# Optimization experiments

Measured on AMD Instinct MI355X. Metric: run time of the kernel, lower is better.

## Reference

```python
import jax, jax.numpy as jnp
import numpy as np
import math

NUM_HEADS = 16
HIDDEN = 1024
HEAD_DIM = HIDDEN // NUM_HEADS
WIN = 512  # relative position window size
B, S = 2, 2048
LN_EPS = 1e-5


def setup_inputs() -> dict:
    key = jax.random.key(0)
    ks = jax.random.split(key, 8)
    sd = 1.0 / math.sqrt(HIDDEN)
    return {
        "x": jax.random.normal(ks[0], (B, S, HIDDEN), jnp.float32),
        "Wq": jax.random.normal(ks[1], (HIDDEN, HIDDEN), jnp.float32) * sd,
        "bq": jnp.zeros((HIDDEN,), jnp.float32),
        "Wk": jax.random.normal(ks[2], (HIDDEN, HIDDEN), jnp.float32) * sd,
        "bk": jnp.zeros((HIDDEN,), jnp.float32),
        "Wv": jax.random.normal(ks[3], (HIDDEN, HIDDEN), jnp.float32) * sd,
        "bv": jnp.zeros((HIDDEN,), jnp.float32),
        "Wo": jax.random.normal(ks[4], (HIDDEN, HIDDEN), jnp.float32) * sd,
        "bo": jnp.zeros((HIDDEN,), jnp.float32),
        "relpos_table": jax.random.normal(ks[5], (WIN, HIDDEN), jnp.float32),
        "ln_gamma": jnp.ones((HIDDEN,), jnp.float32),
        "ln_beta": jnp.zeros((HIDDEN,), jnp.float32),
        "Wrk": jax.random.normal(ks[6], (HIDDEN, HIDDEN), jnp.float32) * sd,
        "brk": jnp.zeros((HIDDEN,), jnp.float32),
        "Wrq": jax.random.normal(ks[7], (HIDDEN, HIDDEN), jnp.float32) * sd,
        "brq": jnp.zeros((HIDDEN,), jnp.float32),
    }


def reference(x, Wq, bq, Wk, bk, Wv, bv, Wo, bo,
              relpos_table, ln_gamma, ln_beta, Wrk, brk, Wrq, brq):
    Bsz, Slen, H = x.shape
    nh, hd = NUM_HEADS, HEAD_DIM

    # QKV projections -> [B, S, nh, hd]
    q = (x @ Wq + bq).reshape(Bsz, Slen, nh, hd)
    k = (x @ Wk + bk).reshape(Bsz, Slen, nh, hd)
    v = (x @ Wv + bv).reshape(Bsz, Slen, nh, hd)

    mu = relpos_table.mean(-1, keepdims=True)
    var = relpos_table.var(-1, keepdims=True)  # biased, as in torch LayerNorm
    e = (relpos_table - mu) * jax.lax.rsqrt(var + LN_EPS) * ln_gamma + ln_beta

    # relative position index matrix [S, S]: clamp(key - query, -W+1, 0) + W-1
    qi = jnp.arange(Slen)
    relpos = jnp.clip(qi[None, :] - qi[:, None], -WIN + 1, 0) + (WIN - 1)

    rk = (e @ Wrk + brk).reshape(WIN, nh, hd)
    rq = (e @ Wrq + brq).reshape(WIN, nh, hd)

    # content-to-content scores [B, nh, S, S]
    c2c = jnp.einsum('bqhd,bkhd->bhqk', q, k)

    # content-to-position: scores over window then gather along window axis
    qps = jnp.einsum('bnhd,whd->bhnw', q, rk)           # [B, nh, S, W]
    c2p = qps[:, :, qi[:, None], relpos]                # [B, nh, S, S]

    # position-to-content: window x key_seq scores, gather along window axis
    kps = jnp.einsum('bnhd,whd->bhwn', k, rq)           # [B, nh, W, S]
    p2c = kps[:, :, relpos, qi[None, :]]                # [B, nh, S, S]

    scale_factor = 3.0  # 1 + relpos_q_enabled + relpos_k_enabled
    logits = (c2c + c2p + p2c) / math.sqrt(hd * scale_factor)

    # causal mask
    causal = qi[None, :] <= qi[:, None]
    logits = jnp.where(causal[None, None], logits, jnp.finfo(logits.dtype).min)

    attn = jax.nn.softmax(logits, axis=-1)              # [B, nh, S, S]
    out = jnp.einsum('bhqk,bkhd->bqhd', attn, v).reshape(Bsz, Slen, H)
    return out @ Wo + bo
```

## Files before the change

kernel.cpp:

```cpp
#include <hip/hip_runtime.h>
#include <math.h>

#define NH 16
#define HD 64
#define HID 1024
#define SEQ 2048
#define NB 2

typedef __attribute__((ext_vector_type(8))) short short8;
typedef __attribute__((ext_vector_type(4))) float f32x4;
typedef unsigned short u16;
typedef unsigned int u32;

constexpr float LN_EPS_C = 1e-5f;
constexpr float SM_SCALE = 0.07216878364870323f;

__device__ inline u16 f2b(float f) {
  unsigned u = __builtin_bit_cast(unsigned, f);
  u = (u + 0x7FFFu + ((u >> 16) & 1u)) >> 16;
  return (u16)u;
}
__device__ inline float b2f(u16 h) {
  unsigned u = ((unsigned)h) << 16;
  return __builtin_bit_cast(float, u);
}
__device__ inline u32 pk2(float lo, float hi) {
  return (u32)f2b(lo) | ((u32)f2b(hi) << 16);
}
__device__ inline f32x4 mfma16(short8 a, short8 b, f32x4 c) {
  return __builtin_amdgcn_mfma_f32_16x16x32_bf16(a, b, c, 0, 0, 0);
}
__device__ inline short8 swz8(const u16* base, int row, int hc) {
  return *reinterpret_cast<const short8*>(&base[row * 64 + 8 * (hc ^ (row & 7))]);
}
__device__ inline int vrot(int row, int col) {
  return row * 72 + ((col + 16 * ((row >> 3) & 3)) & 63);
}
template <int N>
__device__ inline float rorf(float x) {
  return __builtin_bit_cast(float,
      __builtin_amdgcn_update_dpp(0, __builtin_bit_cast(int, x),
                                  0x120 + N, 0xF, 0xF, true));
}
__device__ inline float rmax16(float x) {
  x = fmaxf(x, rorf<1>(x)); x = fmaxf(x, rorf<2>(x));
  x = fmaxf(x, rorf<4>(x)); x = fmaxf(x, rorf<8>(x));
  return x;
}
__device__ inline float rsum16(float x) {
  x += rorf<1>(x); x += rorf<2>(x); x += rorf<4>(x); x += rorf<8>(x);
  return x;
}

__global__ __launch_bounds__(256) void ln_kernel(const float* __restrict__ tbl,
    const float* __restrict__ gamma, const float* __restrict__ beta,
    u16* __restrict__ e) {
  int row = blockIdx.x;
  int t = threadIdx.x;
  const float4* rp = reinterpret_cast<const float4*>(tbl + (size_t)row * HID);
  float4 x = rp[t];
  float s = x.x + x.y + x.z + x.w;
  float ss = x.x * x.x + x.y * x.y + x.z * x.z + x.w * x.w;
  #pragma unroll
  for (int o = 1; o < 64; o <<= 1) {
    s += __shfl_xor(s, o);
    ss += __shfl_xor(ss, o);
  }
  __shared__ float sb[4], ssb[4];
  int w = t >> 6;
  if ((t & 63) == 0) { sb[w] = s; ssb[w] = ss; }
  __syncthreads();
  s = sb[0] + sb[1] + sb[2] + sb[3];
  ss = ssb[0] + ssb[1] + ssb[2] + ssb[3];
  float mu = s * (1.0f / HID);
  float var = ss * (1.0f / HID) - mu * mu;
  float rs = rsqrtf(var + LN_EPS_C);
  float4 g = reinterpret_cast<const float4*>(gamma)[t];
  float4 bt = reinterpret_cast<const float4*>(beta)[t];
  ushort4 o4;
  o4.x = f2b((x.x - mu) * rs * g.x + bt.x);
  o4.y = f2b((x.y - mu) * rs * g.y + bt.y);
  o4.z = f2b((x.z - mu) * rs * g.z + bt.z);
  o4.w = f2b((x.w - mu) * rs * g.w + bt.w);
  *reinterpret_cast<ushort4*>(&e[(size_t)row * HID + t * 4]) = o4;
}

__global__ __launch_bounds__(256) void conv_bf16(const float* __restrict__ src,
    u16* __restrict__ dst, int n) {
  int i = (blockIdx.x * 256 + threadIdx.x) * 8;
  if (i >= n) return;
  float4 a = *reinterpret_cast<const float4*>(&src[i]);
  float4 c = *reinterpret_cast<const float4*>(&src[i + 4]);
  short8 o;
  o[0] = (short)f2b(a.x); o[1] = (short)f2b(a.y); o[2] = (short)f2b(a.z); o[3] = (short)f2b(a.w);
  o[4] = (short)f2b(c.x); o[5] = (short)f2b(c.y); o[6] = (short)f2b(c.z); o[7] = (short)f2b(c.w);
  *reinterpret_cast<short8*>(&dst[i]) = o;
}

struct P6 {
  const float* s[6];
  u16* d[6];
};
__global__ __launch_bounds__(256) void transp_all(P6 p) {
  __shared__ float T[32][33];
  const float* W = p.s[blockIdx.z];
  u16* Wt = p.d[blockIdx.z];
  int bn = blockIdx.x * 32, bk = blockIdx.y * 32;
  int t = threadIdx.x;
  int r = t >> 3, c4 = (t & 7) * 4;
  float4 v = *reinterpret_cast<const float4*>(&W[(size_t)(bk + r) * HID + bn + c4]);
  T[r][c4 + 0] = v.x; T[r][c4 + 1] = v.y; T[r][c4 + 2] = v.z; T[r][c4 + 3] = v.w;
  __syncthreads();
  int n = t >> 3, k4 = (t & 7) * 4;
  ushort4 o;
  o.x = f2b(T[k4 + 0][n]); o.y = f2b(T[k4 + 1][n]);
  o.z = f2b(T[k4 + 2][n]); o.w = f2b(T[k4 + 3][n]);
  *reinterpret_cast<ushort4*>(&Wt[(size_t)(bn + n) * HID + bk + k4]) = o;
}

struct GO {
  const float* bias[3];
  void* out[3];
};
template <bool F32OUT>
__global__ __launch_bounds__(512) void gemm_bf16(const u16* __restrict__ A,
    const u16* __restrict__ Bt, GO go) {
  __shared__ u16 Al[8192];
  __shared__ u16 Bl[8192];
  int t = threadIdx.x;
  int cb = blockIdx.x * 128, rb = blockIdx.y * 128;
  int which = cb >> 10, cbl = cb & 1023;
  const float* bias = go.bias[which];
  void* Cout = go.out[which];
  int wv = t >> 6, lane = t & 63, l15 = lane & 15, lg = lane >> 4;
  int wr = (wv >> 2) * 64, wc = (wv & 3) * 32;
  int srow = t >> 2, sch = t & 3;
  f32x4 acc[4][2];
  #pragma unroll
  for (int i = 0; i < 4; ++i)
    #pragma unroll
    for (int j = 0; j < 2; ++j) acc[i][j] = (f32x4){0.f, 0.f, 0.f, 0.f};
  const u16* Ap = A + (size_t)(rb + srow) * HID;
  const u16* Bp = Bt + (size_t)(cb + srow) * HID;
  int slot0 = 8 * (sch ^ (srow & 7));
  int slot1 = 8 * ((sch + 4) ^ (srow & 7));
  short8 pa0 = *reinterpret_cast<const short8*>(&Ap[sch * 8]);
  short8 pa1 = *reinterpret_cast<const short8*>(&Ap[(sch + 4) * 8]);
  short8 pb0 = *reinterpret_cast<const short8*>(&Bp[sch * 8]);
  short8 pb1 = *reinterpret_cast<const short8*>(&Bp[(sch + 4) * 8]);
  for (int kk = 0; kk < HID; kk += 64) {
    __syncthreads();
    *reinterpret_cast<short8*>(&Al[srow * 64 + slot0]) = pa0;
    *reinterpret_cast<short8*>(&Al[srow * 64 + slot1]) = pa1;
    *reinterpret_cast<short8*>(&Bl[srow * 64 + slot0]) = pb0;
    *reinterpret_cast<short8*>(&Bl[srow * 64 + slot1]) = pb1;
    __syncthreads();
    if (kk + 64 < HID) {
      pa0 = *reinterpret_cast<const short8*>(&Ap[kk + 64 + sch * 8]);
      pa1 = *reinterpret_cast<const short8*>(&Ap[kk + 64 + (sch + 4) * 8]);
      pb0 = *reinterpret_cast<const short8*>(&Bp[kk + 64 + sch * 8]);
      pb1 = *reinterpret_cast<const short8*>(&Bp[kk + 64 + (sch + 4) * 8]);
    }
    #pragma unroll
    for (int s = 0; s < 2; ++s) {
      short8 am[4], bn[2];
      #pragma unroll
      for (int i = 0; i < 4; ++i) am[i] = swz8(Al, wr + i * 16 + l15, s * 4 + lg);
      #pragma unroll
      for (int j = 0; j < 2; ++j) bn[j] = swz8(Bl, wc + j * 16 + l15, s * 4 + lg);
      #pragma unroll
      for (int i = 0; i < 4; ++i)
        #pragma unroll
        for (int j = 0; j < 2; ++j)
          acc[i][j] = mfma16(am[i], bn[j], acc[i][j]);
    }
  }
  #pragma unroll
  for (int j = 0; j < 2; ++j) {
    float bv = bias[cbl + wc + j * 16 + l15];
    #pragma unroll
    for (int i = 0; i < 4; ++i) {
      #pragma unroll
      for (int r = 0; r < 4; ++r) {
        size_t idx = (size_t)(rb + wr + i * 16 + lg * 4 + r) * HID + cbl + wc + j * 16 + l15;
        float v = acc[i][j][r] + bv;
        if (F32OUT) reinterpret_cast<float*>(Cout)[idx] = v;
        else reinterpret_cast<u16*>(Cout)[idx] = f2b(v);
      }
    }
  }
}

__global__ __launch_bounds__(256) void biasqk(const u16* __restrict__ Qb,
    const u16* __restrict__ Kb, const u16* __restrict__ RKb,
    const u16* __restrict__ RQb, float* __restrict__ qrk0,
    float* __restrict__ krq0) {
  int o = blockIdx.x * 64 + (threadIdx.x >> 2);
  int sub = threadIdx.x & 3;
  int b = o >> 15, h = (o >> 11) & 15, i = o & 2047;
  size_t rbase = (size_t)(b * SEQ + i) * HID + h * HD + sub * 16;
  size_t tbase = (size_t)h * HD + sub * 16;
  float s1 = 0.f, s2 = 0.f;
  #pragma unroll
  for (int c = 0; c < 2; ++c) {
    short8 qv = *reinterpret_cast<const short8*>(&Qb[rbase + c * 8]);
    short8 rv = *reinterpret_cast<const short8*>(&RKb[tbase + c * 8]);
    short8 kv = *reinterpret_cast<const short8*>(&Kb[rbase + c * 8]);
    short8 uv = *reinterpret_cast<const short8*>(&RQb[tbase + c * 8]);
    #pragma unroll
    for (int j = 0; j < 8; ++j) {
      s1 += b2f((u16)qv[j]) * b2f((u16)rv[j]);
      s2 += b2f((u16)kv[j]) * b2f((u16)uv[j]);
    }
  }
  s1 += __shfl_xor(s1, 1); s1 += __shfl_xor(s1, 2);
  s2 += __shfl_xor(s2, 1); s2 += __shfl_xor(s2, 2);
  if (sub == 0) { qrk0[o] = s1 * SM_SCALE; krq0[o] = s2 * SM_SCALE; }
}

__global__ __launch_bounds__(256, 3) void bias_kernel(
    const u16* __restrict__ Qb, const u16* __restrict__ Kb,
    const u16* __restrict__ RKb, const u16* __restrict__ RQb,
    u16* __restrict__ bandT) {
  __shared__ u16 smem[20992];
  const int KsO = 0, UO = 4096;
  const int RKO = UO, RQO = UO + 8192;
  const int G1O = UO, G2O = UO + 8448;

  int qt = blockIdx.x;
  int h = blockIdx.y, b = blockIdx.z;
  int q0 = qt * 64;
  int t = threadIdx.x;
  int wv = t >> 6, lane = t & 63, l15 = lane & 15, lg = lane >> 4;
  int qs = q0 + wv * 16;
  int hoff = h * HD;

  size_t qgrow = (size_t)(b * SEQ + qs + l15) * HID + hoff;
  short8 aq0 = *reinterpret_cast<const short8*>(&Qb[qgrow + lg * 8]);
  short8 aq1 = *reinterpret_cast<const short8*>(&Qb[qgrow + 32 + lg * 8]);

  const f32x4 Z = (f32x4){0.f, 0.f, 0.f, 0.f};
  int vr = t >> 2, vc8 = (t & 3) * 8;
  int ktlo = qt - 8; if (ktlo < 0) ktlo = 0;
  size_t tbase = (((size_t)(b * NH + h) * 32 + qt) * 9) << 12;

  for (int kt = ktlo; kt <= qt; ++kt) {
    int k0 = kt * 64;
    int dt = qt - kt;
    int wlo = 448 - 64 * dt; if (wlo < 0) wlo = 0;
    __syncthreads();
    {
      const u16* kg = &Kb[(size_t)(b * SEQ + k0 + vr) * HID + hoff];
      int c0 = vc8 >> 3;
      *reinterpret_cast<short8*>(&smem[KsO + vr * 64 + 8 * (c0 ^ (vr & 7))]) =
          *reinterpret_cast<const short8*>(&kg[vc8]);
      *reinterpret_cast<short8*>(&smem[KsO + vr * 64 + 8 * ((c0 + 4) ^ (vr & 7))]) =
          *reinterpret_cast<const short8*>(&kg[vc8 + 32]);
    }
    for (int e2 = t; e2 < 1024; e2 += 256) {
      int rr = e2 >> 3, cch = e2 & 7;
      int wr2 = wlo + rr; if (wr2 > 511) wr2 = 511;
      size_t gb = (size_t)wr2 * HID + hoff + cch * 8;
      int slot = 8 * (cch ^ (rr & 7));
      *reinterpret_cast<short8*>(&smem[RKO + rr * 64 + slot]) =
          *reinterpret_cast<const short8*>(&RKb[gb]);
      *reinterpret_cast<short8*>(&smem[RQO + rr * 64 + slot]) =
          *reinterpret_cast<const short8*>(&RQb[gb]);
    }
    __syncthreads();
    u32 g1p[16], g2p[16];
    #pragma unroll
    for (int cw = 0; cw < 8; ++cw) {
      short8 r0 = swz8(&smem[RKO], cw * 16 + l15, lg);
      short8 r1 = swz8(&smem[RKO], cw * 16 + l15, 4 + lg);
      f32x4 g = mfma16(r1, aq1, mfma16(r0, aq0, Z));
      g1p[2 * cw] = pk2(g[0], g[1]);
      g1p[2 * cw + 1] = pk2(g[2], g[3]);
    }
    short8 kw0 = swz8(&smem[KsO], wv * 16 + l15, lg);
    short8 kw1 = swz8(&smem[KsO], wv * 16 + l15, 4 + lg);
    #pragma unroll
    for (int cw = 0; cw < 8; ++cw) {
      short8 u0 = swz8(&smem[RQO], cw * 16 + l15, lg);
      short8 u1 = swz8(&smem[RQO], cw * 16 + l15, 4 + lg);
      f32x4 g = mfma16(u1, kw1, mfma16(u0, kw0, Z));
      g2p[2 * cw] = pk2(g[0], g[1]);
      g2p[2 * cw + 1] = pk2(g[2], g[3]);
    }
    __syncthreads();
    #pragma unroll
    for (int cw = 0; cw < 8; ++cw) {
      *reinterpret_cast<uint2*>(&smem[G1O + (wv * 16 + l15) * 132 + cw * 16 + lg * 4]) =
          make_uint2(g1p[2 * cw], g1p[2 * cw + 1]);
      *reinterpret_cast<uint2*>(&smem[G2O + (wv * 16 + l15) * 132 + cw * 16 + lg * 4]) =
          make_uint2(g2p[2 * cw], g2p[2 * cw + 1]);
    }
    __syncthreads();
    u16* outp = bandT + tbase + ((size_t)dt << 12) + t * 16;
    #pragma unroll
    for (int c = 0; c < 4; ++c) {
      float vv[4];
      #pragma unroll
      for (int r = 0; r < 4; ++r) {
        int q = qs + lg * 4 + r;
        int k = k0 + c * 16 + l15;
        int wi = 511 - (q - k) - wlo; if (wi < 0) wi = 0;
        vv[r] = (b2f(smem[G1O + (wv * 16 + lg * 4 + r) * 132 + wi]) +
                 b2f(smem[G2O + (c * 16 + l15) * 132 + wi])) * SM_SCALE;
      }
      *reinterpret_cast<uint2*>(outp + c * 4) =
          make_uint2(pk2(vv[0], vv[1]), pk2(vv[2], vv[3]));
    }
  }
}

__global__ __launch_bounds__(256, 2) void attn_mfma(
    const u16* __restrict__ Qb, const u16* __restrict__ Kb,
    const u16* __restrict__ Vb, const float* __restrict__ qrk0,
    const float* __restrict__ krq0, const u16* __restrict__ bandT,
    u16* __restrict__ ATT) {
  __shared__ u16 smem[22016];
  const int KsB[2] = {0, 4096};
  const int VtB[2] = {8192, 12800};
  const int PsO = 17408;

  int qtA = 31 - (int)blockIdx.x;
  int qtB = (int)blockIdx.x;
  int h = blockIdx.y, b = blockIdx.z;
  int t = threadIdx.x;
  int wv = t >> 6, lane = t & 63, l15 = lane & 15, lg = lane >> 4;
  int hoff = h * HD;
  int bh = (b * NH + h) * SEQ;
  size_t tbaseA = (((size_t)(b * NH + h) * 32 + qtA) * 9) << 12;
  size_t tbaseB = (((size_t)(b * NH + h) * 32 + qtB) * 9) << 12;

  int qsA = qtA * 64 + wv * 16;
  int qsB = qtB * 64 + wv * 16;
  size_t qgA = (size_t)(b * SEQ + qsA + l15) * HID + hoff;
  size_t qgB = (size_t)(b * SEQ + qsB + l15) * HID + hoff;
  short8 aqA0 = *reinterpret_cast<const short8*>(&Qb[qgA + lg * 8]);
  short8 aqA1 = *reinterpret_cast<const short8*>(&Qb[qgA + 32 + lg * 8]);
  short8 aqB0 = *reinterpret_cast<const short8*>(&Qb[qgB + lg * 8]);
  short8 aqB1 = *reinterpret_cast<const short8*>(&Qb[qgB + 32 + lg * 8]);
  float qb0A[4], qb0B[4];
  #pragma unroll
  for (int r = 0; r < 4; ++r) {
    qb0A[r] = qrk0[bh + qsA + lg * 4 + r];
    qb0B[r] = qrk0[bh + qsB + lg * 4 + r];
  }

  float mA[4], lA[4], mB[4], lB[4];
  f32x4 oA[4], oB[4];
  #pragma unroll
  for (int r = 0; r < 4; ++r) { mA[r] = -INFINITY; lA[r] = 0.f; mB[r] = -INFINITY; lB[r] = 0.f; }
  #pragma unroll
  for (int c = 0; c < 4; ++c) {
    oA[c] = (f32x4){0.f, 0.f, 0.f, 0.f};
    oB[c] = (f32x4){0.f, 0.f, 0.f, 0.f};
  }

  const f32x4 Z = (f32x4){0.f, 0.f, 0.f, 0.f};
  int vr = t >> 2, vc8 = (t & 3) * 8;
  int c0s = vc8 >> 3;
  int kslot0 = vr * 64 + 8 * (c0s ^ (vr & 7));
  int kslot1 = vr * 64 + 8 * ((c0s + 4) ^ (vr & 7));
  int vslot[16];
  #pragma unroll
  for (int j = 0; j < 8; ++j) {
    vslot[j] = vrot(vc8 + j, vr);
    vslot[8 + j] = vrot(vc8 + 32 + j, vr);
  }

  {
    const u16* kg = &Kb[(size_t)(b * SEQ + vr) * HID + hoff];
    short8 k0v = *reinterpret_cast<const short8*>(&kg[vc8]);
    short8 k1v = *reinterpret_cast<const short8*>(&kg[vc8 + 32]);
    *reinterpret_cast<short8*>(&smem[KsB[0] + kslot0]) = k0v;
    *reinterpret_cast<short8*>(&smem[KsB[0] + kslot1]) = k1v;
    const u16* vg = &Vb[(size_t)(b * SEQ + vr) * HID + hoff];
    short8 v0v = *reinterpret_cast<const short8*>(&vg[vc8]);
    short8 v1v = *reinterpret_cast<const short8*>(&vg[vc8 + 32]);
    #pragma unroll
    for (int j = 0; j < 8; ++j) smem[VtB[0] + vslot[j]] = (u16)v0v[j];
    #pragma unroll
    for (int j = 0; j < 8; ++j) smem[VtB[0] + vslot[8 + j]] = (u16)v1v[j];
  }
  __syncthreads();

  int cur = 0;
  for (int kt = 0; kt <= qtA; ++kt) {
    int k0 = kt * 64;
    int dtA = qtA - kt;
    bool doB = (kt <= qtB);
    int dtB = qtB - kt;
    bool bandedA = (dtA <= 8);
    bool bandedB = doB && (dtB <= 8);
    int ksb = KsB[cur], vtb = VtB[cur];
    int ksn = KsB[cur ^ 1], vtn = VtB[cur ^ 1];

    short8 pA0, pA1, pB0, pB1;
    if (bandedA) {
      const u16* tb = bandT + tbaseA + ((size_t)dtA << 12) + t * 16;
      pA0 = *reinterpret_cast<const short8*>(tb);
      pA1 = *reinterpret_cast<const short8*>(tb + 8);
    }
    if (bandedB) {
      const u16* tb = bandT + tbaseB + ((size_t)dtB << 12) + t * 16;
      pB0 = *reinterpret_cast<const short8*>(tb);
      pB1 = *reinterpret_cast<const short8*>(tb + 8);
    }
    float kq[4];
    if (dtA > 8 || (doB && dtB > 8)) {
      #pragma unroll
      for (int c = 0; c < 4; ++c) kq[c] = krq0[bh + k0 + c * 16 + l15];
    }
    short8 nk0, nk1, nv0, nv1;
    if (kt < qtA) {
      const u16* kg = &Kb[(size_t)(b * SEQ + k0 + 64 + vr) * HID + hoff];
      nk0 = *reinterpret_cast<const short8*>(&kg[vc8]);
      nk1 = *reinterpret_cast<const short8*>(&kg[vc8 + 32]);
      const u16* vg = &Vb[(size_t)(b * SEQ + k0 + 64 + vr) * HID + hoff];
      nv0 = *reinterpret_cast<const short8*>(&vg[vc8]);
      nv1 = *reinterpret_cast<const short8*>(&vg[vc8 + 32]);
    }

    short8 kb0[4], kb1[4];
    #pragma unroll
    for (int c = 0; c < 4; ++c) {
      kb0[c] = swz8(&smem[ksb], c * 16 + l15, lg);
      kb1[c] = swz8(&smem[ksb], c * 16 + l15, 4 + lg);
    }
    f32x4 sA[4], sB[4];
    #pragma unroll
    for (int c = 0; c < 4; ++c)
      sA[c] = mfma16(aqA1, kb1[c], mfma16(aqA0, kb0[c], Z));
    if (doB) {
      #pragma unroll
      for (int c = 0; c < 4; ++c)
        sB[c] = mfma16(aqB1, kb1[c], mfma16(aqB0, kb0[c], Z));
    }
    #pragma unroll
    for (int c = 0; c < 4; ++c) {
      #pragma unroll
      for (int r = 0; r < 4; ++r) {
        float bbv = bandedA ? b2f((u16)((c < 2 ? pA0 : pA1)[(c & 1) * 4 + r]))
                            : qb0A[r] + kq[c];
        float v = fmaf(sA[c][r], SM_SCALE, bbv);
        if (dtA == 0) {
          int ql = wv * 16 + lg * 4 + r, kl = c * 16 + l15;
          if (ql < kl) v = -INFINITY;
        }
        sA[c][r] = v;
      }
    }
    if (doB) {
      #pragma unroll
      for (int c = 0; c < 4; ++c) {
        #pragma unroll
        for (int r = 0; r < 4; ++r) {
          float bbv = bandedB ? b2f((u16)((c < 2 ? pB0 : pB1)[(c & 1) * 4 + r]))
                              : qb0B[r] + kq[c];
          float v = fmaf(sB[c][r], SM_SCALE, bbv);
          if (dtB == 0) {
            int ql = wv * 16 + lg * 4 + r, kl = c * 16 + l15;
            if (ql < kl) v = -INFINITY;
          }
          sB[c][r] = v;
        }
      }
    }
    float alA[4], alB[4];
    #pragma unroll
    for (int r = 0; r < 4; ++r) {
      float mx = fmaxf(fmaxf(sA[0][r], sA[1][r]), fmaxf(sA[2][r], sA[3][r]));
      mx = rmax16(mx);
      float mn = fmaxf(mA[r], mx);
      alA[r] = __expf(mA[r] - mn);
      float ps = 0.f;
      #pragma unroll
      for (int c = 0; c < 4; ++c) {
        float p = __expf(sA[c][r] - mn);
        sA[c][r] = p;
        ps += p;
      }
      ps = rsum16(ps);
      lA[r] = lA[r] * alA[r] + ps;
      mA[r] = mn;
    }
    if (doB) {
      #pragma unroll
      for (int r = 0; r < 4; ++r) {
        float mx = fmaxf(fmaxf(sB[0][r], sB[1][r]), fmaxf(sB[2][r], sB[3][r]));
        mx = rmax16(mx);
        float mn = fmaxf(mB[r], mx);
        alB[r] = __expf(mB[r] - mn);
        float ps = 0.f;
        #pragma unroll
        for (int c = 0; c < 4; ++c) {
          float p = __expf(sB[c][r] - mn);
          sB[c][r] = p;
          ps += p;
        }
        ps = rsum16(ps);
        lB[r] = lB[r] * alB[r] + ps;
        mB[r] = mn;
      }
    }
    short8 vb0[4], vb1[4];
    #pragma unroll
    for (int c = 0; c < 4; ++c) {
      int n = c * 16 + l15;
      vb0[c] = *reinterpret_cast<const short8*>(&smem[vtb + vrot(n, lg * 8)]);
      vb1[c] = *reinterpret_cast<const short8*>(&smem[vtb + vrot(n, 32 + lg * 8)]);
    }
    #pragma unroll
    for (int c = 0; c < 4; ++c) {
      #pragma unroll
      for (int r = 0; r < 4; ++r) {
        smem[PsO + vrot(wv * 16 + lg * 4 + r, c * 16 + l15)] = f2b(sA[c][r]);
        oA[c][r] *= alA[r];
      }
    }
    int prow = wv * 16 + l15;
    {
      short8 ap0 = *reinterpret_cast<const short8*>(&smem[PsO + vrot(prow, lg * 8)]);
      short8 ap1 = *reinterpret_cast<const short8*>(&smem[PsO + vrot(prow, 32 + lg * 8)]);
      #pragma unroll
      for (int c = 0; c < 4; ++c)
        oA[c] = mfma16(ap1, vb1[c], mfma16(ap0, vb0[c], oA[c]));
    }
    if (doB) {
      #pragma unroll
      for (int c = 0; c < 4; ++c) {
        #pragma unroll
        for (int r = 0; r < 4; ++r) {
          smem[PsO + vrot(wv * 16 + lg * 4 + r, c * 16 + l15)] = f2b(sB[c][r]);
          oB[c][r] *= alB[r];
        }
      }
      short8 bp0 = *reinterpret_cast<const short8*>(&smem[PsO + vrot(prow, lg * 8)]);
      short8 bp1 = *reinterpret_cast<const short8*>(&smem[PsO + vrot(prow, 32 + lg * 8)]);
      #pragma unroll
      for (int c = 0; c < 4; ++c)
        oB[c] = mfma16(bp1, vb1[c], mfma16(bp0, vb0[c], oB[c]));
    }
    if (kt < qtA) {
      *reinterpret_cast<short8*>(&smem[ksn + kslot0]) = nk0;
      *reinterpret_cast<short8*>(&smem[ksn + kslot1]) = nk1;
      #pragma unroll
      for (int j = 0; j < 8; ++j) smem[vtn + vslot[j]] = (u16)nv0[j];
      #pragma unroll
      for (int j = 0; j < 8; ++j) smem[vtn + vslot[8 + j]] = (u16)nv1[j];
    }
    __syncthreads();
    cur ^= 1;
  }
  #pragma unroll
  for (int r = 0; r < 4; ++r) { lA[r] = 1.0f / lA[r]; lB[r] = 1.0f / lB[r]; }
  #pragma unroll
  for (int c = 0; c < 4; ++c) {
    #pragma unroll
    for (int r = 0; r < 4; ++r) {
      size_t obA = (size_t)(b * SEQ + qsA + lg * 4 + r) * HID + hoff + c * 16 + l15;
      ATT[obA] = f2b(oA[c][r] * lA[r]);
      size_t obB = (size_t)(b * SEQ + qsB + lg * 4 + r) * HID + hoff + c * 16 + l15;
      ATT[obB] = f2b(oB[c][r] * lB[r]);
    }
  }
}

extern "C" void kernel_launch(void* const* d_in, const int* in_sizes, int n_in,
                              void* d_out, int out_size, void* d_ws, size_t ws_size,
                              hipStream_t stream) {
  const float* x      = (const float*)d_in[0];
  const float* Wq     = (const float*)d_in[1];
  const float* bq     = (const float*)d_in[2];
  const float* Wk     = (const float*)d_in[3];
  const float* bk     = (const float*)d_in[4];
  const float* Wv     = (const float*)d_in[5];
  const float* bv     = (const float*)d_in[6];
  const float* Wo     = (const float*)d_in[7];
  const float* bo     = (const float*)d_in[8];
  const float* relpos = (const float*)d_in[9];
  const float* gamma  = (const float*)d_in[10];
  const float* beta   = (const float*)d_in[11];
  const float* Wrk    = (const float*)d_in[12];
  const float* brk    = (const float*)d_in[13];
  const float* Wrq    = (const float*)d_in[14];
  const float* brq    = (const float*)d_in[15];
  float* out = (float*)d_out;

  u16* wsu = (u16*)d_ws;
  size_t off = 0;
  auto alloc = [&](size_t n) { u16* p = wsu + off; off += n; return p; };
  u16* xb   = alloc(4194304);
  u16* Eb   = alloc(524288);
  u16* WtQ  = alloc(1048576);
  u16* WtK  = alloc(1048576);
  u16* WtV  = alloc(1048576);
  u16* WtO  = alloc(1048576);
  u16* WtRK = alloc(1048576);
  u16* WtRQ = alloc(1048576);
  u16* Qb2  = alloc(4194304);
  u16* Kb2  = alloc(4194304);
  u16* Vb2  = alloc(4194304);
  u16* ATTb = alloc(4194304);
  u16* RKb2 = alloc(524288);
  u16* RQb2 = alloc(524288);
  float* qrk0 = (float*)(wsu + off); off += 131072;
  float* krq0 = (float*)(wsu + off); off += 131072;
  u16* bandT = alloc((size_t)NB * NH * 32 * 9 * 4096);

  ln_kernel<<<512, 256, 0, stream>>>(relpos, gamma, beta, Eb);
  conv_bf16<<<2048, 256, 0, stream>>>(x, xb, 4194304);
  P6 p6;
  p6.s[0] = Wq; p6.s[1] = Wk; p6.s[2] = Wv; p6.s[3] = Wo; p6.s[4] = Wrk; p6.s[5] = Wrq;
  p6.d[0] = WtQ; p6.d[1] = WtK; p6.d[2] = WtV; p6.d[3] = WtO; p6.d[4] = WtRK; p6.d[5] = WtRQ;
  dim3 gT(32, 32, 6);
  transp_all<<<gT, 256, 0, stream>>>(p6);

  GO goQKV = {{bq, bk, bv}, {Qb2, Kb2, Vb2}};
  dim3 gQKV(24, 32);
  gemm_bf16<false><<<gQKV, 512, 0, stream>>>(xb, WtQ, goQKV);
  GO goRel = {{brk, brq, brq}, {RKb2, RQb2, RQb2}};
  dim3 gRel2(16, 4);
  gemm_bf16<false><<<gRel2, 512, 0, stream>>>(Eb, WtRK, goRel);

  biasqk<<<1024, 256, 0, stream>>>(Qb2, Kb2, RKb2, RQb2, qrk0, krq0);

  dim3 gB(32, NH, NB);
  bias_kernel<<<gB, 256, 0, stream>>>(Qb2, Kb2, RKb2, RQb2, bandT);

  dim3 gA(16, NH, NB);
  attn_mfma<<<gA, 256, 0, stream>>>(Qb2, Kb2, Vb2, qrk0, krq0, bandT, ATTb);

  GO goOut = {{bo, bo, bo}, {out, out, out}};
  dim3 gBig(8, 32);
  gemm_bf16<true><<<gBig, 512, 0, stream>>>(ATTb, WtO, goOut);
}
```

Measured before the change: 218.9 us.

## Split attention key loop across two blocks and merge partial softmax results

Each attention block now handles every other key tile, selected by a split index taken from blockIdx.x, so the attention grid doubles from 512 to 1024 blocks. Each block writes unnormalized fp32 partial outputs plus its per-row max and sum to a workspace buffer. A new merge kernel combines the two halves with a log-sum-exp rescale and writes the bf16 attention output. The aim is more blocks in flight for better CU occupancy and latency hiding, at the cost of extra global traffic for the fp32 partials and one more kernel launch.

```diff
diff --git a/kernel.cpp b/kernel.cpp
--- a/kernel.cpp
+++ b/kernel.cpp
@@ -318,14 +318,16 @@
     const u16* __restrict__ Qb, const u16* __restrict__ Kb,
     const u16* __restrict__ Vb, const float* __restrict__ qrk0,
     const float* __restrict__ krq0, const u16* __restrict__ bandT,
-    u16* __restrict__ ATT) {
+    float* __restrict__ part) {
   __shared__ u16 smem[22016];
   const int KsB[2] = {0, 4096};
   const int VtB[2] = {8192, 12800};
   const int PsO = 17408;
 
-  int qtA = 31 - (int)blockIdx.x;
-  int qtB = (int)blockIdx.x;
+  int pr = (int)blockIdx.x >> 1;
+  int sp = (int)blockIdx.x & 1;
+  int qtA = 31 - pr;
+  int qtB = pr;
   int h = blockIdx.y, b = blockIdx.z;
   int t = threadIdx.x;
   int wv = t >> 6, lane = t & 63, l15 = lane & 15, lg = lane >> 4;
@@ -372,12 +374,12 @@
   }
 
   {
-    const u16* kg = &Kb[(size_t)(b * SEQ + vr) * HID + hoff];
+    const u16* kg = &Kb[(size_t)(b * SEQ + sp * 64 + vr) * HID + hoff];
     short8 k0v = *reinterpret_cast<const short8*>(&kg[vc8]);
     short8 k1v = *reinterpret_cast<const short8*>(&kg[vc8 + 32]);
     *reinterpret_cast<short8*>(&smem[KsB[0] + kslot0]) = k0v;
     *reinterpret_cast<short8*>(&smem[KsB[0] + kslot1]) = k1v;
-    const u16* vg = &Vb[(size_t)(b * SEQ + vr) * HID + hoff];
+    const u16* vg = &Vb[(size_t)(b * SEQ + sp * 64 + vr) * HID + hoff];
     short8 v0v = *reinterpret_cast<const short8*>(&vg[vc8]);
     short8 v1v = *reinterpret_cast<const short8*>(&vg[vc8 + 32]);
     #pragma unroll
@@ -388,7 +390,7 @@
   __syncthreads();
 
   int cur = 0;
-  for (int kt = 0; kt <= qtA; ++kt) {
+  for (int kt = sp; kt <= qtA; kt += 2) {
     int k0 = kt * 64;
     int dtA = qtA - kt;
     bool doB = (kt <= qtB);
@@ -415,11 +417,11 @@
       for (int c = 0; c < 4; ++c) kq[c] = krq0[bh + k0 + c * 16 + l15];
     }
     short8 nk0, nk1, nv0, nv1;
-    if (kt < qtA) {
-      const u16* kg = &Kb[(size_t)(b * SEQ + k0 + 64 + vr) * HID + hoff];
+    if (kt + 2 <= qtA) {
+      const u16* kg = &Kb[(size_t)(b * SEQ + k0 + 128 + vr) * HID + hoff];
       nk0 = *reinterpret_cast<const short8*>(&kg[vc8]);
       nk1 = *reinterpret_cast<const short8*>(&kg[vc8 + 32]);
-      const u16* vg = &Vb[(size_t)(b * SEQ + k0 + 64 + vr) * HID + hoff];
+      const u16* vg = &Vb[(size_t)(b * SEQ + k0 + 128 + vr) * HID + hoff];
       nv0 = *reinterpret_cast<const short8*>(&vg[vc8]);
       nv1 = *reinterpret_cast<const short8*>(&vg[vc8 + 32]);
     }
@@ -544,7 +546,7 @@
       for (int c = 0; c < 4; ++c)
         oB[c] = mfma16(bp1, vb1[c], mfma16(bp0, vb0[c], oB[c]));
     }
-    if (kt < qtA) {
+    if (kt + 2 <= qtA) {
       *reinterpret_cast<short8*>(&smem[ksn + kslot0]) = nk0;
       *reinterpret_cast<short8*>(&smem[ksn + kslot1]) = nk1;
       #pragma unroll
@@ -555,17 +557,52 @@
     __syncthreads();
     cur ^= 1;
   }
-  #pragma unroll
-  for (int r = 0; r < 4; ++r) { lA[r] = 1.0f / lA[r]; lB[r] = 1.0f / lB[r]; }
+  size_t pbA = ((((size_t)(b * NH + h)) * 32 + qtA) * 2 + sp) * 4224;
+  size_t pbB = ((((size_t)(b * NH + h)) * 32 + qtB) * 2 + sp) * 4224;
   #pragma unroll
   for (int c = 0; c < 4; ++c) {
     #pragma unroll
     for (int r = 0; r < 4; ++r) {
-      size_t obA = (size_t)(b * SEQ + qsA + lg * 4 + r) * HID + hoff + c * 16 + l15;
-      ATT[obA] = f2b(oA[c][r] * lA[r]);
-      size_t obB = (size_t)(b * SEQ + qsB + lg * 4 + r) * HID + hoff + c * 16 + l15;
-      ATT[obB] = f2b(oB[c][r] * lB[r]);
-    }
+      int row = wv * 16 + lg * 4 + r;
+      part[pbA + row * 64 + c * 16 + l15] = oA[c][r];
+      part[pbB + row * 64 + c * 16 + l15] = oB[c][r];
+    }
+  }
+  if (l15 == 0) {
+    #pragma unroll
+    for (int r = 0; r < 4; ++r) {
+      int row = wv * 16 + lg * 4 + r;
+      part[pbA + 4096 + row] = mA[r];
+      part[pbA + 4160 + row] = lA[r];
+      part[pbB + 4096 + row] = mB[r];
+      part[pbB + 4160 + row] = lB[r];
+    }
+  }
+}
+
+__global__ __launch_bounds__(256) void attn_merge(const float* __restrict__ part,
+    u16* __restrict__ ATT) {
+  int qt = blockIdx.x, h = blockIdx.y, b = blockIdx.z;
+  int t = threadIdx.x;
+  int row = t >> 2, c0 = (t & 3) * 16;
+  size_t p0 = ((((size_t)(b * NH + h)) * 32 + qt) * 2) * 4224;
+  size_t p1 = p0 + 4224;
+  float m0 = part[p0 + 4096 + row], l0 = part[p0 + 4160 + row];
+  float m1 = part[p1 + 4096 + row], l1 = part[p1 + 4160 + row];
+  float mm = fmaxf(m0, m1);
+  float a0 = __expf(m0 - mm), a1 = __expf(m1 - mm);
+  float li = 1.0f / (l0 * a0 + l1 * a1);
+  size_t ob = (size_t)(b * SEQ + qt * 64 + row) * HID + h * HD + c0;
+  #pragma unroll
+  for (int j4 = 0; j4 < 4; ++j4) {
+    float4 v0 = *reinterpret_cast<const float4*>(&part[p0 + row * 64 + c0 + j4 * 4]);
+    float4 v1 = *reinterpret_cast<const float4*>(&part[p1 + row * 64 + c0 + j4 * 4]);
+    ushort4 o4;
+    o4.x = f2b((v0.x * a0 + v1.x * a1) * li);
+    o4.y = f2b((v0.y * a0 + v1.y * a1) * li);
+    o4.z = f2b((v0.z * a0 + v1.z * a1) * li);
+    o4.w = f2b((v0.w * a0 + v1.w * a1) * li);
+    *reinterpret_cast<ushort4*>(&ATT[ob + j4 * 4]) = o4;
   }
 }
 
@@ -610,6 +647,7 @@
   float* qrk0 = (float*)(wsu + off); off += 131072;
   float* krq0 = (float*)(wsu + off); off += 131072;
   u16* bandT = alloc((size_t)NB * NH * 32 * 9 * 4096);
+  float* part = (float*)(wsu + off); off += (size_t)NB * NH * 32 * 2 * 4224 * 2;
 
   ln_kernel<<<512, 256, 0, stream>>>(relpos, gamma, beta, Eb);
   conv_bf16<<<2048, 256, 0, stream>>>(x, xb, 4194304);
@@ -631,8 +669,9 @@
   dim3 gB(32, NH, NB);
   bias_kernel<<<gB, 256, 0, stream>>>(Qb2, Kb2, RKb2, RQb2, bandT);
 
-  dim3 gA(16, NH, NB);
-  attn_mfma<<<gA, 256, 0, stream>>>(Qb2, Kb2, Vb2, qrk0, krq0, bandT, ATTb);
+  dim3 gA(32, NH, NB);
+  attn_mfma<<<gA, 256, 0, stream>>>(Qb2, Kb2, Vb2, qrk0, krq0, bandT, part);
+  attn_merge<<<gB, 256, 0, stream>>>(part, ATTb);
 
   GO goOut = {{bo, bo, bo}, {out, out, out}};
   dim3 gBig(8, 32);
```

After: 229.5 us. 1.05x slower.
